# Kernel tuning notes

Hardware: AMD Instinct MI355X
Metric: run time of the kernel (lower is better)

## Reference

```python
import jax, jax.numpy as jnp
from jax import lax
import numpy as np

H = 512      # hidden_size
NF = 64      # nfeatures
NL = 2       # num_layers
OUT = 1      # output_size
B, T = 64, 512


def _uniform(key, shape, scale):
    return jax.random.uniform(key, shape, jnp.float32, -scale, scale)


def setup_inputs() -> dict:
    key = jax.random.key(0)
    ks = jax.random.split(key, 12)
    s = 1.0 / np.sqrt(H)  # PyTorch LSTM/Linear init scale
    return {
        "x": jax.random.normal(ks[0], (B, T, NF), jnp.float32),
        # layer 0 (input NF -> H), PyTorch gate order i,f,g,o along 4H axis
        "W_ih0": _uniform(ks[1], (4 * H, NF), s),
        "W_hh0": _uniform(ks[2], (4 * H, H), s),
        "b_ih0": _uniform(ks[3], (4 * H,), s),
        "b_hh0": _uniform(ks[4], (4 * H,), s),
        # layer 1 (input H -> H)
        "W_ih1": _uniform(ks[5], (4 * H, H), s),
        "W_hh1": _uniform(ks[6], (4 * H, H), s),
        "b_ih1": _uniform(ks[7], (4 * H,), s),
        "b_hh1": _uniform(ks[8], (4 * H,), s),
        # final linear head
        "W_fc": _uniform(ks[9], (OUT, H), s),
        "b_fc": _uniform(ks[10], (OUT,), s),
    }


def _lstm_layer(x, W_ih, W_hh, b_ih, b_hh):
    """x: [B, T, D_in] -> hidden sequence [B, T, H]. Zero initial state."""
    b, t, _ = x.shape
    h0 = jnp.zeros((b, H), x.dtype)
    c0 = jnp.zeros((b, H), x.dtype)
    # precompute input projections for all timesteps: [T, B, 4H]
    xp = jnp.swapaxes(jnp.einsum('btd,gd->btg', x, W_ih) + b_ih + b_hh, 0, 1)

    def step(carry, xt):
        h, c = carry
        gates = xt + h @ W_hh.T  # [B, 4H]
        i, f, g, o = jnp.split(gates, 4, axis=-1)
        i = jax.nn.sigmoid(i)
        f = jax.nn.sigmoid(f)
        g = jnp.tanh(g)
        o = jax.nn.sigmoid(o)
        c = f * c + i * g
        h = o * jnp.tanh(c)
        return (h, c), h

    _, hs = lax.scan(step, (h0, c0), xp)  # hs: [T, B, H]
    return jnp.swapaxes(hs, 0, 1)


def reference(x, W_ih0, W_hh0, b_ih0, b_hh0, W_ih1, W_hh1, b_ih1, b_hh1, W_fc, b_fc):
    h = _lstm_layer(x, W_ih0, W_hh0, b_ih0, b_hh0)
    h = _lstm_layer(h, W_ih1, W_hh1, b_ih1, b_hh1)
    return h @ W_fc.T + b_fc  # [B, T, OUT]
```

## Files before the change

### kernel.cpp

```cpp
#include <hip/hip_runtime.h>

#define T_STEPS 512
#define BATCH   64
#define HID     512

typedef __attribute__((ext_vector_type(8))) short short8;
typedef __attribute__((ext_vector_type(4))) float f32x4;

__device__ __forceinline__ unsigned short f2bf(float f){
  unsigned u = __float_as_uint(f);
  u += 0x7FFF + ((u >> 16) & 1);
  return (unsigned short)(u >> 16);
}
__device__ __forceinline__ float bf2f(unsigned short s){
  return __uint_as_float(((unsigned)s) << 16);
}
__device__ __forceinline__ f32x4 mfma16(short8 a, short8 b, f32x4 c){
  return __builtin_amdgcn_mfma_f32_16x16x32_bf16(a, b, c, 0, 0, 0);
}
__device__ __forceinline__ float sigf(float x){
  return 1.0f / (1.0f + exp2f(-1.44269504f * x));
}
__device__ __forceinline__ float tanh_(float x){
  float e = exp2f(2.88539008f * x);
  return 1.0f - 2.0f / (1.0f + e);
}

__device__ __forceinline__ void spinL0(int* flags0, int target){
  int lane = threadIdx.x & 63;
  int* p = &flags0[(lane & 31)*32];
  float a0 = 1.0f;
  int guard = 0;
  for (;;){
    int v = __hip_atomic_load(p, __ATOMIC_RELAXED, __HIP_MEMORY_SCOPE_AGENT);
    if (__ballot(v >= target) == ~0ull) break;
    #pragma unroll
    for (int i = 0; i < 8; ++i) a0 = __builtin_fmaf(a0, 1.000001f, 0.000001f);
    if (++guard > (1 << 18)) break;
  }
  asm volatile("" :: "v"(a0));
  asm volatile("" ::: "memory");
  __builtin_amdgcn_fence(__ATOMIC_ACQUIRE, "workgroup");
}

__device__ __forceinline__ void spinL1(int* flags0, int* flags1, int t){
  int lane = threadIdx.x & 63;
  int* p   = (lane < 32) ? &flags0[lane*32] : &flags1[(lane-32)*32];
  int tgt  = (lane < 32) ? t + 1 : t;
  float a0 = 1.0f;
  int guard = 0;
  for (;;){
    int v = __hip_atomic_load(p, __ATOMIC_RELAXED, __HIP_MEMORY_SCOPE_AGENT);
    if (__ballot(v >= tgt) == ~0ull) break;
    #pragma unroll
    for (int i = 0; i < 8; ++i) a0 = __builtin_fmaf(a0, 1.000001f, 0.000001f);
    if (++guard > (1 << 18)) break;
  }
  asm volatile("" :: "v"(a0));
  asm volatile("" ::: "memory");
  __builtin_amdgcn_fence(__ATOMIC_ACQUIRE, "workgroup");
}

__device__ __forceinline__ void signalSlot(int* slot, int val){
  __builtin_amdgcn_fence(__ATOMIC_RELEASE, "workgroup");
  asm volatile("" ::: "memory");
  __hip_atomic_store(slot, val, __ATOMIC_RELAXED, __HIP_MEMORY_SCOPE_AGENT);
}

template<int NKB>
__device__ __forceinline__ void loadB(const unsigned short* __restrict__ Wg, int K, int kstart,
                                      int l15, int l4, short8 B[4][NKB]){
  #pragma unroll
  for (int tt = 0; tt < 4; ++tt)
    #pragma unroll
    for (int kb = 0; kb < NKB; ++kb)
      B[tt][kb] = *(const short8*)(Wg + (long)(tt*16 + l15)*K + kstart + kb*32 + l4*8);
}

template<int NKB>
__device__ __forceinline__ void gemmA(const unsigned short* __restrict__ Ab, long rs,
                                      int l15, int l4, const short8 B[4][NKB], f32x4 acc[4][4]){
  #pragma unroll
  for (int kb = 0; kb < NKB; ++kb){
    short8 a[4];
    #pragma unroll
    for (int m = 0; m < 4; ++m)
      a[m] = *(const short8*)(Ab + (long)(m*16 + l15)*rs + kb*32 + l4*8);
    #pragma unroll
    for (int m = 0; m < 4; ++m)
      #pragma unroll
      for (int tt = 0; tt < 4; ++tt)
        acc[m][tt] = mfma16(B[tt][kb], a[m], acc[m][tt]);
  }
}

__device__ __forceinline__ void reduceWrite(float* red, int w, int l15, int l4, f32x4 acc[4][4]){
  #pragma unroll
  for (int m = 0; m < 4; ++m){
    if (m == w) continue;
    int mi = (m > w) ? m - 1 : m;
    #pragma unroll
    for (int tt = 0; tt < 4; ++tt){
      float* p = red + (w*12 + mi*4 + tt)*320 + l15*20 + l4*4;
      *(f32x4*)p = acc[m][tt];
    }
  }
}
__device__ __forceinline__ void reduceRead(const float* red, int w, int l15, int l4,
                                           f32x4 gf[4], f32x4 acc[4][4]){
  #pragma unroll
  for (int tt = 0; tt < 4; ++tt) gf[tt] = acc[w][tt];
  #pragma unroll
  for (int v = 0; v < 4; ++v){
    if (v == w) continue;
    int mi = (w > v) ? w - 1 : w;
    #pragma unroll
    for (int tt = 0; tt < 4; ++tt){
      const float* p = red + (v*12 + mi*4 + tt)*320 + l15*20 + l4*4;
      gf[tt] += *(const f32x4*)p;
    }
  }
}

__device__ __forceinline__ void gatesStore(f32x4 gf[4], f32x4& cst,
                                           unsigned short* __restrict__ hdst){
  f32x4 hh;
  #pragma unroll
  for (int r = 0; r < 4; ++r){
    float iv = sigf(gf[0][r]), fv = sigf(gf[1][r]);
    float gv = tanh_(gf[2][r]), ov = sigf(gf[3][r]);
    float cv = fv * cst[r] + iv * gv;
    cst[r] = cv;
    hh[r] = ov * tanh_(cv);
  }
  unsigned long long pk = (unsigned long long)f2bf(hh[0])
    | ((unsigned long long)f2bf(hh[1]) << 16)
    | ((unsigned long long)f2bf(hh[2]) << 32)
    | ((unsigned long long)f2bf(hh[3]) << 48);
  __hip_atomic_store((unsigned long long*)hdst, pk, __ATOMIC_RELAXED, __HIP_MEMORY_SCOPE_AGENT);
}

template<int NXB, int NHB>
__device__ void l0_loop(int g, int w, int lane,
                        const unsigned short* __restrict__ Wg,
                        const float* __restrict__ bias0,
                        const unsigned short* __restrict__ xb,
                        unsigned short* __restrict__ h0seq,
                        int* flags0, float* red, int hk0){
  int l15 = lane & 15, l4 = lane >> 4;
  short8 Bx[4][(NXB > 0) ? NXB : 1];
  if constexpr (NXB > 0) loadB<NXB>(Wg, 576, 0, l15, l4, Bx);
  short8 Bh[4][NHB];
  loadB<NHB>(Wg, 576, 64 + hk0, l15, l4, Bh);
  f32x4 bsv[4];
  #pragma unroll
  for (int tt = 0; tt < 4; ++tt) bsv[tt] = *(const f32x4*)&bias0[(g*4 + tt)*16 + l4*4];
  f32x4 cst = {0.f, 0.f, 0.f, 0.f};
  int b = w*16 + l15, colb = g*16 + l4*4;

  for (int t = 0; t < T_STEPS; ++t){
    f32x4 acc[4][4];
    #pragma unroll
    for (int m = 0; m < 4; ++m)
      #pragma unroll
      for (int tt = 0; tt < 4; ++tt) acc[m][tt] = (f32x4){0.f,0.f,0.f,0.f};
    if constexpr (NXB > 0)
      gemmA<NXB>(xb + (long)t*64, (long)T_STEPS*64, l15, l4, Bx, acc);
    if (t){
      spinL0(flags0, t);
      gemmA<NHB>(h0seq + (long)(t-1)*BATCH*HID + hk0, HID, l15, l4, Bh, acc);
    }
    reduceWrite(red, w, l15, l4, acc);
    __syncthreads();
    f32x4 gf[4];
    reduceRead(red, w, l15, l4, gf, acc);
    #pragma unroll
    for (int tt = 0; tt < 4; ++tt) gf[tt] += bsv[tt];
    gatesStore(gf, cst, h0seq + (long)t*BATCH*HID + (long)b*HID + colb);
    __syncthreads();
    if (threadIdx.x == 0) signalSlot(&flags0[g*32], t + 1);
  }
}

__device__ void l1_loop(int g, int w, int lane,
                        const unsigned short* __restrict__ Wg,
                        const float* __restrict__ bias1,
                        const unsigned short* __restrict__ h0seq,
                        unsigned short* __restrict__ h1seq,
                        int* flags0, int* flags1, float* red){
  int l15 = lane & 15, l4 = lane >> 4;
  short8 Bh[4][8];
  loadB<8>(Wg, 1024, w*256, l15, l4, Bh);
  f32x4 bsv[4];
  #pragma unroll
  for (int tt = 0; tt < 4; ++tt) bsv[tt] = *(const f32x4*)&bias1[(g*4 + tt)*16 + l4*4];
  f32x4 cst = {0.f, 0.f, 0.f, 0.f};
  int b = w*16 + l15, colb = g*16 + l4*4;

  for (int t = 0; t < T_STEPS; ++t){
    spinL1(flags0, flags1, t);
    f32x4 acc[4][4];
    #pragma unroll
    for (int m = 0; m < 4; ++m)
      #pragma unroll
      for (int tt = 0; tt < 4; ++tt) acc[m][tt] = (f32x4){0.f,0.f,0.f,0.f};
    if (w < 2)
      gemmA<8>(h0seq + (long)t*BATCH*HID + w*256, HID, l15, l4, Bh, acc);
    else if (t)
      gemmA<8>(h1seq + (long)(t-1)*BATCH*HID + (w-2)*256, HID, l15, l4, Bh, acc);
    reduceWrite(red, w, l15, l4, acc);
    __syncthreads();
    f32x4 gf[4];
    reduceRead(red, w, l15, l4, gf, acc);
    #pragma unroll
    for (int tt = 0; tt < 4; ++tt) gf[tt] += bsv[tt];
    gatesStore(gf, cst, h1seq + (long)t*BATCH*HID + (long)b*HID + colb);
    __syncthreads();
    if (threadIdx.x == 0) signalSlot(&flags1[g*32], t + 1);
  }
}

extern "C" __global__ void __launch_bounds__(256, 1)
lstm_persist(const unsigned short* __restrict__ Wpk0,
             const unsigned short* __restrict__ Wpk1,
             const float* __restrict__ bias0, const float* __restrict__ bias1,
             const unsigned short* __restrict__ xb,
             unsigned short* __restrict__ h0seq, unsigned short* __restrict__ h1seq,
             int* flags0, int* flags1){
  __shared__ float red[15360];
  int wg = blockIdx.x;
  int role = wg >> 5;
  int g = wg & 31;
  int w = threadIdx.x >> 6;
  int lane = threadIdx.x & 63;

  if (role == 0){
    const unsigned short* Wg = Wpk0 + (long)g*4*16*576;
    switch (w){
      case 0:  l0_loop<2,3>(g, 0, lane, Wg, bias0, xb, h0seq, flags0, red, 0);   break;
      case 1:  l0_loop<0,5>(g, 1, lane, Wg, bias0, xb, h0seq, flags0, red, 96);  break;
      case 2:  l0_loop<0,4>(g, 2, lane, Wg, bias0, xb, h0seq, flags0, red, 256); break;
      default: l0_loop<0,4>(g, 3, lane, Wg, bias0, xb, h0seq, flags0, red, 384); break;
    }
  } else {
    const unsigned short* Wg = Wpk1 + (long)g*4*16*1024;
    l1_loop(g, w, lane, Wg, bias1, h0seq, h1seq, flags0, flags1, red);
  }
}

extern "C" __global__ void prep_kernel(const float* __restrict__ x,
    const float* __restrict__ Wih0, const float* __restrict__ Whh0,
    const float* __restrict__ bih0, const float* __restrict__ bhh0,
    const float* __restrict__ Wih1, const float* __restrict__ Whh1,
    const float* __restrict__ bih1, const float* __restrict__ bhh1,
    unsigned short* __restrict__ Wpk0, unsigned short* __restrict__ Wpk1,
    float* __restrict__ bias0, float* __restrict__ bias1,
    unsigned short* __restrict__ xb, int* __restrict__ syncm){
  long gid = (long)blockIdx.x * blockDim.x + threadIdx.x;
  long gs  = (long)gridDim.x * blockDim.x;
  const long NW0 = 32L*4*16*576;
  const long NW1 = 32L*4*16*1024;
  const long NX  = 64L*512*64;

  for (long i = gid; i < NW0; i += gs){
    int k = (int)(i % 576);
    long q = i / 576;
    int r  = (int)(q & 15);
    long q2 = q >> 4;
    int tt = (int)(q2 & 3);
    int g  = (int)(q2 >> 2);
    int row = tt*512 + g*16 + r;
    float v = (k < 64) ? Wih0[(long)row*64 + k] : Whh0[(long)row*512 + (k - 64)];
    Wpk0[i] = f2bf(v);
  }
  for (long i = gid; i < NW1; i += gs){
    int k = (int)(i & 1023);
    long q = i >> 10;
    int r  = (int)(q & 15);
    long q2 = q >> 4;
    int tt = (int)(q2 & 3);
    int g  = (int)(q2 >> 2);
    int row = tt*512 + g*16 + r;
    float v = (k < 512) ? Wih1[(long)row*512 + k] : Whh1[(long)row*512 + (k - 512)];
    Wpk1[i] = f2bf(v);
  }
  for (long i = gid; i < 2048; i += gs){
    int r = (int)(i & 15);
    int tt = (int)((i >> 4) & 3);
    int g  = (int)(i >> 6);
    int row = tt*512 + g*16 + r;
    bias0[i] = bih0[row] + bhh0[row];
    bias1[i] = bih1[row] + bhh1[row];
  }
  for (long i = gid; i < NX; i += gs) xb[i] = f2bf(x[i]);
  for (long i = gid; i < 2048; i += gs) syncm[i] = 0;
}

extern "C" __global__ void head_kernel(const unsigned short* __restrict__ h1seq,
    const float* __restrict__ wfc, const float* __restrict__ bfc,
    float* __restrict__ out){
  int t = blockIdx.x;
  int tid = threadIdx.x;
  int b = tid >> 2, q = tid & 3;
  const unsigned short* hp = h1seq + ((long)t*BATCH + b)*HID + q*128;
  const float* wp = wfc + q*128;
  float s = 0.f;
  #pragma unroll
  for (int i = 0; i < 16; ++i){
    short8 v = *(const short8*)(hp + i*8);
    #pragma unroll
    for (int e = 0; e < 8; ++e)
      s += bf2f((unsigned short)v[e]) * wp[i*8 + e];
  }
  s += __shfl_xor(s, 1, 64);
  s += __shfl_xor(s, 2, 64);
  if (q == 0) out[(long)b*T_STEPS + t] = s + bfc[0];
}

extern "C" void kernel_launch(void* const* d_in, const int* in_sizes, int n_in,
                              void* d_out, int out_size, void* d_ws, size_t ws_size,
                              hipStream_t stream){
  const float* x    = (const float*)d_in[0];
  const float* Wih0 = (const float*)d_in[1];
  const float* Whh0 = (const float*)d_in[2];
  const float* bih0 = (const float*)d_in[3];
  const float* bhh0 = (const float*)d_in[4];
  const float* Wih1 = (const float*)d_in[5];
  const float* Whh1 = (const float*)d_in[6];
  const float* bih1 = (const float*)d_in[7];
  const float* bhh1 = (const float*)d_in[8];
  const float* wfc  = (const float*)d_in[9];
  const float* bfc  = (const float*)d_in[10];
  float* out = (float*)d_out;

  char* p = (char*)d_ws;
  auto carve = [&](size_t bytes) -> void* {
    void* r = (void*)p;
    p += (bytes + 255) & ~(size_t)255;
    return r;
  };
  unsigned short* Wpk0  = (unsigned short*)carve(32L*4*16*576*2);
  unsigned short* Wpk1  = (unsigned short*)carve(32L*4*16*1024*2);
  float* bias0 = (float*)carve(2048*4);
  float* bias1 = (float*)carve(2048*4);
  unsigned short* xb    = (unsigned short*)carve(64L*512*64*2);
  unsigned short* h0seq = (unsigned short*)carve(512L*64*512*2);
  unsigned short* h1seq = (unsigned short*)carve(512L*64*512*2);
  int* syncm   = (int*)carve(8192);
  int* flags0 = syncm;
  int* flags1 = syncm + 1024;

  hipLaunchKernelGGL(prep_kernel, dim3(1024), dim3(256), 0, stream,
                     x, Wih0, Whh0, bih0, bhh0, Wih1, Whh1, bih1, bhh1,
                     Wpk0, Wpk1, bias0, bias1, xb, syncm);
  hipLaunchKernelGGL(lstm_persist, dim3(64), dim3(256), 0, stream,
                     Wpk0, Wpk1, bias0, bias1, xb, h0seq, h1seq, flags0, flags1);
  hipLaunchKernelGGL(head_kernel, dim3(512), dim3(256), 0, stream,
                     h1seq, wfc, bfc, out);
}
```

Baseline: 5.174 ms.

## Replace block barrier signaling with per-wave flags and widen spin filler

Each wave now publishes its own progress flag after its stores drain, instead of the whole workgroup barrier-syncing and thread 0 signaling once per block. Consumers poll 128 per-wave flags (two loads per lane) rather than 32 per-block ones. This removes one __syncthreads per timestep and lets producers signal as soon as each wave is done. The spin loop's dummy FMA filler is enlarged to four chains, which lowers polling pressure but can add wake-up latency. The flag buffer and its zeroing grow to match.

```diff
diff --git a/kernel.cpp b/kernel.cpp
--- a/kernel.cpp
+++ b/kernel.cpp
@@ -26,45 +26,64 @@
   return 1.0f - 2.0f / (1.0f + e);
 }
 
+#define SPIN_FILLER(a0,a1,a2,a3)                                              \
+  _Pragma("unroll")                                                           \
+  for (int _i = 0; _i < 32; ++_i){                                            \
+    a0 = __builtin_fmaf(a0, 1.000001f, 1e-7f);                                \
+    a1 = __builtin_fmaf(a1, 1.000001f, 1e-7f);                                \
+    a2 = __builtin_fmaf(a2, 1.000001f, 1e-7f);                                \
+    a3 = __builtin_fmaf(a3, 1.000001f, 1e-7f);                                \
+  }
+
 __device__ __forceinline__ void spinL0(int* flags0, int target){
   int lane = threadIdx.x & 63;
-  int* p = &flags0[(lane & 31)*32];
-  float a0 = 1.0f;
+  int* pa = &flags0[lane*32];
+  int* pb = &flags0[(lane + 64)*32];
+  float a0 = 1.f, a1 = 1.f, a2 = 1.f, a3 = 1.f;
   int guard = 0;
   for (;;){
-    int v = __hip_atomic_load(p, __ATOMIC_RELAXED, __HIP_MEMORY_SCOPE_AGENT);
+    int va = __hip_atomic_load(pa, __ATOMIC_RELAXED, __HIP_MEMORY_SCOPE_AGENT);
+    int vb = __hip_atomic_load(pb, __ATOMIC_RELAXED, __HIP_MEMORY_SCOPE_AGENT);
+    int v = (va < vb) ? va : vb;
     if (__ballot(v >= target) == ~0ull) break;
-    #pragma unroll
-    for (int i = 0; i < 8; ++i) a0 = __builtin_fmaf(a0, 1.000001f, 0.000001f);
+    SPIN_FILLER(a0, a1, a2, a3)
     if (++guard > (1 << 18)) break;
   }
-  asm volatile("" :: "v"(a0));
+  asm volatile("" :: "v"(a0), "v"(a1), "v"(a2), "v"(a3));
   asm volatile("" ::: "memory");
   __builtin_amdgcn_fence(__ATOMIC_ACQUIRE, "workgroup");
 }
 
 __device__ __forceinline__ void spinL1(int* flags0, int* flags1, int t){
   int lane = threadIdx.x & 63;
-  int* p   = (lane < 32) ? &flags0[lane*32] : &flags1[(lane-32)*32];
-  int tgt  = (lane < 32) ? t + 1 : t;
-  float a0 = 1.0f;
+  int* p0 = &flags0[lane*32];
+  int* p1 = &flags0[(lane + 64)*32];
+  int* p2 = &flags1[lane*32];
+  int* p3 = &flags1[(lane + 64)*32];
+  float a0 = 1.f, a1 = 1.f, a2 = 1.f, a3 = 1.f;
   int guard = 0;
   for (;;){
-    int v = __hip_atomic_load(p, __ATOMIC_RELAXED, __HIP_MEMORY_SCOPE_AGENT);
-    if (__ballot(v >= tgt) == ~0ull) break;
-    #pragma unroll
-    for (int i = 0; i < 8; ++i) a0 = __builtin_fmaf(a0, 1.000001f, 0.000001f);
+    int v0 = __hip_atomic_load(p0, __ATOMIC_RELAXED, __HIP_MEMORY_SCOPE_AGENT);
+    int v1 = __hip_atomic_load(p1, __ATOMIC_RELAXED, __HIP_MEMORY_SCOPE_AGENT);
+    int v2 = __hip_atomic_load(p2, __ATOMIC_RELAXED, __HIP_MEMORY_SCOPE_AGENT);
+    int v3 = __hip_atomic_load(p3, __ATOMIC_RELAXED, __HIP_MEMORY_SCOPE_AGENT);
+    int m0 = ((v0 < v1) ? v0 : v1) - (t + 1);
+    int m1 = ((v2 < v3) ? v2 : v3) - t;
+    int v = (m0 < m1) ? m0 : m1;
+    if (__ballot(v >= 0) == ~0ull) break;
+    SPIN_FILLER(a0, a1, a2, a3)
     if (++guard > (1 << 18)) break;
   }
-  asm volatile("" :: "v"(a0));
+  asm volatile("" :: "v"(a0), "v"(a1), "v"(a2), "v"(a3));
   asm volatile("" ::: "memory");
   __builtin_amdgcn_fence(__ATOMIC_ACQUIRE, "workgroup");
 }
 
-__device__ __forceinline__ void signalSlot(int* slot, int val){
+__device__ __forceinline__ void waveSignal(int* slot, int val, int lane){
   __builtin_amdgcn_fence(__ATOMIC_RELEASE, "workgroup");
-  asm volatile("" ::: "memory");
-  __hip_atomic_store(slot, val, __ATOMIC_RELAXED, __HIP_MEMORY_SCOPE_AGENT);
+  asm volatile("s_waitcnt vmcnt(0)" ::: "memory");
+  if (lane == 0)
+    __hip_atomic_store(slot, val, __ATOMIC_RELAXED, __HIP_MEMORY_SCOPE_AGENT);
 }
 
 template<int NKB>
@@ -157,6 +176,7 @@
   for (int tt = 0; tt < 4; ++tt) bsv[tt] = *(const f32x4*)&bias0[(g*4 + tt)*16 + l4*4];
   f32x4 cst = {0.f, 0.f, 0.f, 0.f};
   int b = w*16 + l15, colb = g*16 + l4*4;
+  int* myslot = &flags0[(g*4 + w)*32];
 
   for (int t = 0; t < T_STEPS; ++t){
     f32x4 acc[4][4];
@@ -177,8 +197,7 @@
     #pragma unroll
     for (int tt = 0; tt < 4; ++tt) gf[tt] += bsv[tt];
     gatesStore(gf, cst, h0seq + (long)t*BATCH*HID + (long)b*HID + colb);
-    __syncthreads();
-    if (threadIdx.x == 0) signalSlot(&flags0[g*32], t + 1);
+    waveSignal(myslot, t + 1, lane);
   }
 }
 
@@ -196,6 +215,7 @@
   for (int tt = 0; tt < 4; ++tt) bsv[tt] = *(const f32x4*)&bias1[(g*4 + tt)*16 + l4*4];
   f32x4 cst = {0.f, 0.f, 0.f, 0.f};
   int b = w*16 + l15, colb = g*16 + l4*4;
+  int* myslot = &flags1[(g*4 + w)*32];
 
   for (int t = 0; t < T_STEPS; ++t){
     spinL1(flags0, flags1, t);
@@ -215,8 +235,7 @@
     #pragma unroll
     for (int tt = 0; tt < 4; ++tt) gf[tt] += bsv[tt];
     gatesStore(gf, cst, h1seq + (long)t*BATCH*HID + (long)b*HID + colb);
-    __syncthreads();
-    if (threadIdx.x == 0) signalSlot(&flags1[g*32], t + 1);
+    waveSignal(myslot, t + 1, lane);
   }
 }
 
@@ -293,7 +312,7 @@
     bias1[i] = bih1[row] + bhh1[row];
   }
   for (long i = gid; i < NX; i += gs) xb[i] = f2bf(x[i]);
-  for (long i = gid; i < 2048; i += gs) syncm[i] = 0;
+  for (long i = gid; i < 8192; i += gs) syncm[i] = 0;
 }
 
 extern "C" __global__ void head_kernel(const unsigned short* __restrict__ h1seq,
@@ -346,9 +365,9 @@
   unsigned short* xb    = (unsigned short*)carve(64L*512*64*2);
   unsigned short* h0seq = (unsigned short*)carve(512L*64*512*2);
   unsigned short* h1seq = (unsigned short*)carve(512L*64*512*2);
-  int* syncm   = (int*)carve(8192);
+  int* syncm   = (int*)carve(32768);
   int* flags0 = syncm;
-  int* flags1 = syncm + 1024;
+  int* flags1 = syncm + 4096;
 
   hipLaunchKernelGGL(prep_kernel, dim3(1024), dim3(256), 0, stream,
                      x, Wih0, Whh0, bih0, bhh0, Wih1, Whh1, bih1, bhh1,
```

Result: slower. 6.124 ms (+18.4%).

## Split layer-1 K work across waves and decouple layer-0/layer-1 flag waits

Applied to the files above, without the earlier changes.

Layer-1 previously gave waves 0-1 the input projection and waves 2-3 the recurrent projection, all behind one combined spin on both flag arrays. Now every wave handles a 128-wide slice of both halves: it waits only on the layer-0 flags, runs the input GEMM, then waits on the layer-1 flags before the recurrent GEMM. The layer-1 flag is also prefetched early in the step. The spin loop no longer has the dummy FMA backoff, and each lane caches the last flag value it saw so it stops reloading once satisfied. The intent is to overlap waiting on one dependency with work on the other and to cut polling latency, at the cost of more register pressure and a tighter poll that can add memory traffic.

```diff
diff --git a/kernel.cpp b/kernel.cpp
--- a/kernel.cpp
+++ b/kernel.cpp
@@ -26,37 +26,19 @@
   return 1.0f - 2.0f / (1.0f + e);
 }
 
-__device__ __forceinline__ void spinL0(int* flags0, int target){
+__device__ __forceinline__ int aload(const int* p){
+  return __hip_atomic_load(p, __ATOMIC_RELAXED, __HIP_MEMORY_SCOPE_AGENT);
+}
+
+__device__ __forceinline__ void spinF(int* flags, int target, int& lastv){
   int lane = threadIdx.x & 63;
-  int* p = &flags0[(lane & 31)*32];
-  float a0 = 1.0f;
+  int* p = &flags[(lane & 31)*32];
   int guard = 0;
-  for (;;){
-    int v = __hip_atomic_load(p, __ATOMIC_RELAXED, __HIP_MEMORY_SCOPE_AGENT);
-    if (__ballot(v >= target) == ~0ull) break;
-    #pragma unroll
-    for (int i = 0; i < 8; ++i) a0 = __builtin_fmaf(a0, 1.000001f, 0.000001f);
+  while (__ballot(lastv >= target) != ~0ull){
+    if (lastv < target)
+      lastv = aload(p);
     if (++guard > (1 << 18)) break;
   }
-  asm volatile("" :: "v"(a0));
-  asm volatile("" ::: "memory");
-  __builtin_amdgcn_fence(__ATOMIC_ACQUIRE, "workgroup");
-}
-
-__device__ __forceinline__ void spinL1(int* flags0, int* flags1, int t){
-  int lane = threadIdx.x & 63;
-  int* p   = (lane < 32) ? &flags0[lane*32] : &flags1[(lane-32)*32];
-  int tgt  = (lane < 32) ? t + 1 : t;
-  float a0 = 1.0f;
-  int guard = 0;
-  for (;;){
-    int v = __hip_atomic_load(p, __ATOMIC_RELAXED, __HIP_MEMORY_SCOPE_AGENT);
-    if (__ballot(v >= tgt) == ~0ull) break;
-    #pragma unroll
-    for (int i = 0; i < 8; ++i) a0 = __builtin_fmaf(a0, 1.000001f, 0.000001f);
-    if (++guard > (1 << 18)) break;
-  }
-  asm volatile("" :: "v"(a0));
   asm volatile("" ::: "memory");
   __builtin_amdgcn_fence(__ATOMIC_ACQUIRE, "workgroup");
 }
@@ -157,6 +139,7 @@
   for (int tt = 0; tt < 4; ++tt) bsv[tt] = *(const f32x4*)&bias0[(g*4 + tt)*16 + l4*4];
   f32x4 cst = {0.f, 0.f, 0.f, 0.f};
   int b = w*16 + l15, colb = g*16 + l4*4;
+  int lastv = 0;
 
   for (int t = 0; t < T_STEPS; ++t){
     f32x4 acc[4][4];
@@ -167,7 +150,7 @@
     if constexpr (NXB > 0)
       gemmA<NXB>(xb + (long)t*64, (long)T_STEPS*64, l15, l4, Bx, acc);
     if (t){
-      spinL0(flags0, t);
+      spinF(flags0, t, lastv);
       gemmA<NHB>(h0seq + (long)(t-1)*BATCH*HID + hk0, HID, l15, l4, Bh, acc);
     }
     reduceWrite(red, w, l15, l4, acc);
@@ -189,25 +172,31 @@
                         unsigned short* __restrict__ h1seq,
                         int* flags0, int* flags1, float* red){
   int l15 = lane & 15, l4 = lane >> 4;
-  short8 Bh[4][8];
-  loadB<8>(Wg, 1024, w*256, l15, l4, Bh);
+  short8 Bh0[4][4], Bh1[4][4];
+  loadB<4>(Wg, 1024, w*128,       l15, l4, Bh0);
+  loadB<4>(Wg, 1024, 512 + w*128, l15, l4, Bh1);
   f32x4 bsv[4];
   #pragma unroll
   for (int tt = 0; tt < 4; ++tt) bsv[tt] = *(const f32x4*)&bias1[(g*4 + tt)*16 + l4*4];
   f32x4 cst = {0.f, 0.f, 0.f, 0.f};
   int b = w*16 + l15, colb = g*16 + l4*4;
+  int lastv0 = 0, lastv1 = 0;
+  int* p1 = &flags1[(lane & 31)*32];
 
   for (int t = 0; t < T_STEPS; ++t){
-    spinL1(flags0, flags1, t);
+    int v1pre = (t && lastv1 < t) ? aload(p1) : lastv1;
     f32x4 acc[4][4];
     #pragma unroll
     for (int m = 0; m < 4; ++m)
       #pragma unroll
       for (int tt = 0; tt < 4; ++tt) acc[m][tt] = (f32x4){0.f,0.f,0.f,0.f};
-    if (w < 2)
-      gemmA<8>(h0seq + (long)t*BATCH*HID + w*256, HID, l15, l4, Bh, acc);
-    else if (t)
-      gemmA<8>(h1seq + (long)(t-1)*BATCH*HID + (w-2)*256, HID, l15, l4, Bh, acc);
+    spinF(flags0, t + 1, lastv0);
+    gemmA<4>(h0seq + (long)t*BATCH*HID + w*128, HID, l15, l4, Bh0, acc);
+    if (t){
+      lastv1 = (v1pre > lastv1) ? v1pre : lastv1;
+      spinF(flags1, t, lastv1);
+      gemmA<4>(h1seq + (long)(t-1)*BATCH*HID + w*128, HID, l15, l4, Bh1, acc);
+    }
     reduceWrite(red, w, l15, l4, acc);
     __syncthreads();
     f32x4 gf[4];
```

Result: slower. 5.908 ms (+14.2%).

## Replace block barrier signaling with per-wave atomic counters and batch A loads

Applied to the files above, without the earlier changes.

Removes the trailing __syncthreads before each step's completion flag. Each wave now drains its own stores and atomically increments the group's flag, so consumers wait for a count of 4*t instead of t. Separately, the A-operand loads for the recurrent GEMM are all issued before the MFMAs, so global load latency overlaps instead of being paid per k-block. This costs more registers and more atomic traffic on the flags.

```diff
diff --git a/kernel.cpp b/kernel.cpp
--- a/kernel.cpp
+++ b/kernel.cpp
@@ -43,10 +43,10 @@
   __builtin_amdgcn_fence(__ATOMIC_ACQUIRE, "workgroup");
 }
 
-__device__ __forceinline__ void spinL1(int* flags0, int* flags1, int t){
+__device__ __forceinline__ void spinL1(int* flags0, int* flags1, int tgt0, int tgt1){
   int lane = threadIdx.x & 63;
   int* p   = (lane < 32) ? &flags0[lane*32] : &flags1[(lane-32)*32];
-  int tgt  = (lane < 32) ? t + 1 : t;
+  int tgt  = (lane < 32) ? tgt0 : tgt1;
   float a0 = 1.0f;
   int guard = 0;
   for (;;){
@@ -61,10 +61,11 @@
   __builtin_amdgcn_fence(__ATOMIC_ACQUIRE, "workgroup");
 }
 
-__device__ __forceinline__ void signalSlot(int* slot, int val){
+__device__ __forceinline__ void signalWave(int* slot, int lane){
   __builtin_amdgcn_fence(__ATOMIC_RELEASE, "workgroup");
-  asm volatile("" ::: "memory");
-  __hip_atomic_store(slot, val, __ATOMIC_RELAXED, __HIP_MEMORY_SCOPE_AGENT);
+  asm volatile("s_waitcnt vmcnt(0)" ::: "memory");
+  if (lane == 0)
+    __hip_atomic_fetch_add(slot, 1, __ATOMIC_RELAXED, __HIP_MEMORY_SCOPE_AGENT);
 }
 
 template<int NKB>
@@ -75,6 +76,29 @@
     #pragma unroll
     for (int kb = 0; kb < NKB; ++kb)
       B[tt][kb] = *(const short8*)(Wg + (long)(tt*16 + l15)*K + kstart + kb*32 + l4*8);
+}
+
+template<int NKB>
+__device__ __forceinline__ void loadA(const unsigned short* __restrict__ Ab, long rs,
+                                      int l15, int l4, short8 a[4][NKB]){
+  #pragma unroll
+  for (int m = 0; m < 4; ++m){
+    const unsigned short* pm = Ab + (long)(m*16 + l15)*rs + l4*8;
+    #pragma unroll
+    for (int kb = 0; kb < NKB; ++kb)
+      a[m][kb] = *(const short8*)(pm + kb*32);
+  }
+}
+template<int NKB>
+__device__ __forceinline__ void mfmaA(const short8 a[4][NKB], const short8 B[4][NKB],
+                                      f32x4 acc[4][4]){
+  #pragma unroll
+  for (int kb = 0; kb < NKB; ++kb)
+    #pragma unroll
+    for (int m = 0; m < 4; ++m)
+      #pragma unroll
+      for (int tt = 0; tt < 4; ++tt)
+        acc[m][tt] = mfma16(B[tt][kb], a[m][kb], acc[m][tt]);
 }
 
 template<int NKB>
@@ -167,8 +191,10 @@
     if constexpr (NXB > 0)
       gemmA<NXB>(xb + (long)t*64, (long)T_STEPS*64, l15, l4, Bx, acc);
     if (t){
-      spinL0(flags0, t);
-      gemmA<NHB>(h0seq + (long)(t-1)*BATCH*HID + hk0, HID, l15, l4, Bh, acc);
+      spinL0(flags0, 4*t);
+      short8 ah[4][NHB];
+      loadA<NHB>(h0seq + (long)(t-1)*BATCH*HID + hk0, HID, l15, l4, ah);
+      mfmaA<NHB>(ah, Bh, acc);
     }
     reduceWrite(red, w, l15, l4, acc);
     __syncthreads();
@@ -177,8 +203,7 @@
     #pragma unroll
     for (int tt = 0; tt < 4; ++tt) gf[tt] += bsv[tt];
     gatesStore(gf, cst, h0seq + (long)t*BATCH*HID + (long)b*HID + colb);
-    __syncthreads();
-    if (threadIdx.x == 0) signalSlot(&flags0[g*32], t + 1);
+    signalWave(&flags0[g*32], lane);
   }
 }
 
@@ -198,16 +223,21 @@
   int b = w*16 + l15, colb = g*16 + l4*4;
 
   for (int t = 0; t < T_STEPS; ++t){
-    spinL1(flags0, flags1, t);
+    spinL1(flags0, flags1, 4*(t+1), 4*t);
     f32x4 acc[4][4];
     #pragma unroll
     for (int m = 0; m < 4; ++m)
       #pragma unroll
       for (int tt = 0; tt < 4; ++tt) acc[m][tt] = (f32x4){0.f,0.f,0.f,0.f};
-    if (w < 2)
-      gemmA<8>(h0seq + (long)t*BATCH*HID + w*256, HID, l15, l4, Bh, acc);
-    else if (t)
-      gemmA<8>(h1seq + (long)(t-1)*BATCH*HID + (w-2)*256, HID, l15, l4, Bh, acc);
+    if (w < 2){
+      short8 ah[4][8];
+      loadA<8>(h0seq + (long)t*BATCH*HID + w*256, HID, l15, l4, ah);
+      mfmaA<8>(ah, Bh, acc);
+    } else if (t){
+      short8 ah[4][8];
+      loadA<8>(h1seq + (long)(t-1)*BATCH*HID + (w-2)*256, HID, l15, l4, ah);
+      mfmaA<8>(ah, Bh, acc);
+    }
     reduceWrite(red, w, l15, l4, acc);
     __syncthreads();
     f32x4 gf[4];
@@ -215,8 +245,7 @@
     #pragma unroll
     for (int tt = 0; tt < 4; ++tt) gf[tt] += bsv[tt];
     gatesStore(gf, cst, h1seq + (long)t*BATCH*HID + (long)b*HID + colb);
-    __syncthreads();
-    if (threadIdx.x == 0) signalSlot(&flags1[g*32], t + 1);
+    signalWave(&flags1[g*32], lane);
   }
 }
 
```

Measured after the change: 6.574 ms. 27.1% more time.
